# Kernel optimization log

Hardware: AMD Instinct MI355X
Metric: run time of the kernel (lower is better)

The kernel has to match this reference:

```python
import jax, jax.numpy as jnp
import numpy as np

N_NODES = 100000
N_EDGES = 1600000
IN_CH = 256
OUT_CH = 128
EPS = 1e-12


def setup_inputs() -> dict:
    key = jax.random.key(0)
    k1, k2, k3 = jax.random.split(key, 3)
    x = jax.random.normal(k1, (N_NODES, IN_CH), dtype=jnp.float32)
    edge_index = jax.random.randint(k2, (2, N_EDGES), 0, N_NODES, dtype=jnp.int64)
    W = jax.random.normal(k3, (IN_CH, OUT_CH), dtype=jnp.float32) / np.float32(np.sqrt(IN_CH))
    b = jnp.zeros((OUT_CH,), dtype=jnp.float32)
    return {"x": x, "edge_index": edge_index, "W": W, "b": b}


def reference(x, edge_index, W, b):
    n = x.shape[0]
    # GCNConv: linear transform first, then normalized aggregation with self-loops
    h = x @ W  # [N, out]
    loops = jnp.arange(n, dtype=edge_index.dtype)
    row = jnp.concatenate([edge_index[0], loops])  # source nodes
    col = jnp.concatenate([edge_index[1], loops])  # destination nodes
    deg = jax.ops.segment_sum(jnp.ones_like(col, dtype=h.dtype), col, num_segments=n)
    dinv = jnp.where(deg > 0, jax.lax.rsqrt(jnp.maximum(deg, 1.0)), 0.0)  # deg^-1/2, inf->0
    wgt = dinv[row] * dinv[col]  # symmetric normalization per edge
    agg = jax.ops.segment_sum(h[row] * wgt[:, None], col, num_segments=n) + b  # [N, out]
    # min-max scale per node (dim=1)
    zmin = agg.min(axis=1, keepdims=True)
    zmax = agg.max(axis=1, keepdims=True)
    z = (agg - zmin) / (zmax - zmin)
    # F.normalize: L2 along dim=1 with eps clamp
    nrm = jnp.maximum(jnp.linalg.norm(z, axis=1, keepdims=True), EPS)
    return z / nrm
```

## Files before the change

kernel.cpp:

```cpp
#include <hip/hip_runtime.h>
#include <hip/hip_bf16.h>

#define N_NODES 100000
#define N_EDGES 1600000
#define IN_CH 256
#define OUT_CH 128

#define BSZ 256
#define NBUCK 391
#define BCAP 4736
#define CSC 4096
#define SCB 391
#define PREPB 64

#define GEMM_ROWS 32
#define GEMB 3125

typedef __attribute__((ext_vector_type(8))) short short8;
typedef __attribute__((ext_vector_type(4))) float floatx4;
typedef __attribute__((ext_vector_type(2))) float float2v;

union bfu { __hip_bfloat16 b; unsigned short u; };

__device__ inline unsigned short f2bf(float v) {
    bfu cv; cv.b = __float2bfloat16(v); return cv.u;
}
__device__ inline float bf2f(unsigned short u) {
    bfu cv; cv.u = u; return __bfloat162float(cv.b);
}

__device__ inline void pkfma(float2v& acc, unsigned g, float2v dnp) {
    float2v v;
    v.x = __uint_as_float(g << 16);
    v.y = __uint_as_float(g & 0xffff0000u);
    asm("v_pk_fma_f32 %0, %1, %2, %3" : "=v"(acc) : "v"(v), "v"(dnp), "v"(acc));
}

__global__ __launch_bounds__(512) void k_init(const float* __restrict__ W,
                                              unsigned short* __restrict__ wb_hi,
                                              unsigned short* __restrict__ wb_lo,
                                              int* __restrict__ bcursor,
                                              unsigned* __restrict__ zrow) {
    int tid = threadIdx.x;
    if (blockIdx.x == 0 && tid < NBUCK) bcursor[tid] = 0;
    if (blockIdx.x == 1 && tid < 64) zrow[tid] = 0;

    int t = blockIdx.x * 512 + tid;
    int j = t & 7;
    int lane = (t >> 3) & 63;
    int s = (t >> 9) & 7;
    int nt = t >> 12;
    int k = s * 32 + (lane >> 4) * 8 + j;
    int n = nt * 16 + (lane & 15);
    float w = W[k * OUT_CH + n];
    unsigned short hi = f2bf(w);
    wb_hi[t] = hi;
    wb_lo[t] = f2bf(w - bf2f(hi));
}

__global__ __launch_bounds__(512) void k_main(const int* __restrict__ rows,
                                              const int* __restrict__ cols,
                                              int* __restrict__ bcursor,
                                              unsigned* __restrict__ ebuf,
                                              const float* __restrict__ x,
                                              const unsigned short* __restrict__ wb_hi,
                                              const unsigned short* __restrict__ wb_lo,
                                              unsigned short* __restrict__ hbs) {
    __shared__ int lcnt[NBUCK];
    __shared__ int lbase[NBUCK];
    __shared__ short8 xbh[2 * 8 * 68];
    __shared__ short8 xbl[2 * 8 * 68];

    int t = threadIdx.x;

    if (blockIdx.x < SCB) {
        if (t < NBUCK) lcnt[t] = 0;
        __syncthreads();

        int s0 = blockIdx.x * CSC;
        int e1 = min(N_EDGES, s0 + CSC);

        unsigned val[8];
        int bkr[8], rk[8];
#pragma unroll
        for (int u = 0; u < 8; ++u) {
            int i = s0 + t + u * 512;
            bool p = i < e1;
            int c = p ? cols[i] : 0;
            int r = p ? rows[i] : 0;
            int bk = c >> 8;
            bkr[u] = bk;
            val[u] = ((unsigned)(c & (BSZ - 1)) << 17) | (unsigned)r;
            rk[u] = p ? atomicAdd(&lcnt[bk], 1) : 0;
        }
        __syncthreads();
        if (t < NBUCK) {
            int c = lcnt[t];
            lbase[t] = c ? atomicAdd(&bcursor[t], c) : 0;
        }
        __syncthreads();
#pragma unroll
        for (int u = 0; u < 8; ++u) {
            int i = s0 + t + u * 512;
            if (i < e1) ebuf[bkr[u] * BCAP + lbase[bkr[u]] + rk[u]] = val[u];
        }
        return;
    }

    int wv = t >> 6;
    int lane = t & 63;
    int row0 = (blockIdx.x - SCB) * GEMM_ROWS;

    short8 Bh[8], Bl[8];
    const short8* bhp = (const short8*)wb_hi + (size_t)wv * 8 * 64 + lane;
    const short8* blp = (const short8*)wb_lo + (size_t)wv * 8 * 64 + lane;
#pragma unroll
    for (int s = 0; s < 8; ++s) {
        Bh[s] = bhp[s * 64];
        Bl[s] = blp[s * 64];
    }

#pragma unroll
    for (int q = 0; q < 2; ++q) {
        int c = q * 512 + t;
        int row = c >> 5;
        int cc  = c & 31;
        const float4* xp = (const float4*)(x + (size_t)(row0 + row) * IN_CH + cc * 8);
        float4 v0 = xp[0];
        float4 v1 = xp[1];
        float xv[8] = {v0.x, v0.y, v0.z, v0.w, v1.x, v1.y, v1.z, v1.w};
        short8 hh, ll;
#pragma unroll
        for (int j = 0; j < 8; ++j) {
            unsigned short hi = f2bf(xv[j]);
            hh[j] = (short)hi;
            ll[j] = (short)f2bf(xv[j] - bf2f(hi));
        }
        int ms = row >> 4, r15 = row & 15, s = cc >> 2, q2 = cc & 3;
        int idx = (ms * 8 + s) * 68 + q2 * 17 + r15;
        xbh[idx] = hh;
        xbl[idx] = ll;
    }
    __syncthreads();

    int r15 = lane & 15;
    int quad = lane >> 4;
    int lidx = quad * 17 + r15;

    floatx4 acc[2];
#pragma unroll
    for (int ms = 0; ms < 2; ++ms) {
        acc[ms] = (floatx4){0.f, 0.f, 0.f, 0.f};
#pragma unroll
        for (int s = 0; s < 8; ++s) {
            short8 ah = xbh[(ms * 8 + s) * 68 + lidx];
            short8 al = xbl[(ms * 8 + s) * 68 + lidx];
            acc[ms] = __builtin_amdgcn_mfma_f32_16x16x32_bf16(ah, Bh[s], acc[ms], 0, 0, 0);
            acc[ms] = __builtin_amdgcn_mfma_f32_16x16x32_bf16(ah, Bl[s], acc[ms], 0, 0, 0);
            acc[ms] = __builtin_amdgcn_mfma_f32_16x16x32_bf16(al, Bh[s], acc[ms], 0, 0, 0);
        }
    }

#pragma unroll
    for (int ms = 0; ms < 2; ++ms)
#pragma unroll
        for (int r = 0; r < 4; ++r) {
            int row = row0 + ms * 16 + quad * 4 + r;
            size_t idx = (size_t)row * OUT_CH + wv * 16 + r15;
            hbs[idx] = f2bf(acc[ms][r]);
        }
}

__global__ __launch_bounds__(512) void pb_build(const unsigned* __restrict__ ebuf,
                                                const int* __restrict__ bcursor,
                                                int* __restrict__ cnt,
                                                int* __restrict__ base,
                                                float* __restrict__ dinv,
                                                int* __restrict__ es) {
    __shared__ int nh[BSZ];
    __shared__ int sc[BSZ];
    int t = threadIdx.x;
    int bk = blockIdx.x;
    int bb = bk * BCAP;
    int bc = bcursor[bk];
    if (t < BSZ) nh[t] = 0;
    __syncthreads();

    unsigned val[10];
    int rk[10];
#pragma unroll
    for (int u = 0; u < 10; ++u) {
        int i = t + u * 512;
        bool p = i < bc;
        unsigned v = p ? ebuf[bb + i] : 0u;
        val[u] = v;
        rk[u] = p ? atomicAdd(&nh[v >> 17], 1) : 0;
    }
    __syncthreads();
    if (t < BSZ) sc[t] = nh[t];
    __syncthreads();
    for (int off = 1; off < BSZ; off <<= 1) {
        int v = (t < BSZ && t >= off) ? sc[t - off] : 0;
        __syncthreads();
        if (t < BSZ) sc[t] += v;
        __syncthreads();
    }
    if (t < BSZ) {
        int node = bk * BSZ + t;
        if (node < N_NODES) {
            int c = nh[t];
            cnt[node] = c;
            base[node] = bb + sc[t] - c;
            dinv[node] = rsqrtf((float)(c + 1));
        }
    }
#pragma unroll
    for (int u = 0; u < 10; ++u) {
        int i = t + u * 512;
        if (i < bc) {
            unsigned v = val[u];
            int dl = v >> 17;
            es[bb + sc[dl] - nh[dl] + rk[u]] = (int)(v & 0x1FFFFu) << 8;
        }
    }
}

__global__ __launch_bounds__(256) void k_agg_fin(const unsigned short* __restrict__ hbs,
                                                 const float* __restrict__ dinv,
                                                 const int* __restrict__ es,
                                                 const int* __restrict__ base,
                                                 const int* __restrict__ cnt,
                                                 const float* __restrict__ b,
                                                 float* __restrict__ out) {
    int t = threadIdx.x;
    int lane = t & 63;
    int ll = lane & 15;
    int node = blockIdx.x * 16 + (t >> 4);

    const char* hb = (const char*)hbs;
    const char* dvc = (const char*)dinv;
    int lane_byte = ll << 4;
    int bidx = (lane & 48) << 2;

    float dn = dinv[node];
    int d  = cnt[node];
    int st = base[node];

    float4 bv0 = ((const float4*)b)[ll * 2];
    float4 bv1 = ((const float4*)b)[ll * 2 + 1];

    uint4 gs = *(const uint4*)(hb + ((size_t)node << 8) + lane_byte);
    float2v dself; dself.x = dn; dself.y = dn;
    float2v acc[4];
#pragma unroll
    for (int c = 0; c < 4; ++c) { acc[c].x = 0.f; acc[c].y = 0.f; }
    pkfma(acc[0], gs.x, dself); pkfma(acc[1], gs.y, dself);
    pkfma(acc[2], gs.z, dself); pkfma(acc[3], gs.w, dself);

    int dm = d;
    dm = max(dm, __shfl_xor(dm, 16, 64));
    dm = max(dm, __shfl_xor(dm, 32, 64));
    int iters = __builtin_amdgcn_readfirstlane((dm + 15) >> 4);

    const int zoff = N_NODES << 8;

    int off = zoff; float dnv = 0.f;
    if (ll < d) {
        off = es[st + ll];
        dnv = *(const float*)(dvc + ((unsigned)off >> 6));
    }

    for (int it = 0; it < iters; ++it) {
        int offn = zoff; float dnn = 0.f;
        int jb2 = (it + 1) << 4;
        if (jb2 + ll < d) {
            offn = es[st + jb2 + ll];
            dnn = *(const float*)(dvc + ((unsigned)offn >> 6));
        }
        int dni = __float_as_int(dnv);

        uint4 ga[4], gb[4];
        float2v da[4], db[4];
#pragma unroll
        for (int k = 0; k < 4; ++k) {
            int ro = __builtin_amdgcn_ds_bpermute(bidx + (k << 2), off);
            float f = __int_as_float(__builtin_amdgcn_ds_bpermute(bidx + (k << 2), dni));
            da[k].x = f; da[k].y = f;
            ga[k] = *(const uint4*)(hb + (unsigned)(ro + lane_byte));
        }
#pragma unroll
        for (int k = 0; k < 4; ++k) {
            int ro = __builtin_amdgcn_ds_bpermute(bidx + ((4 + k) << 2), off);
            float f = __int_as_float(__builtin_amdgcn_ds_bpermute(bidx + ((4 + k) << 2), dni));
            db[k].x = f; db[k].y = f;
            gb[k] = *(const uint4*)(hb + (unsigned)(ro + lane_byte));
        }
#pragma unroll
        for (int k = 0; k < 4; ++k) {
            pkfma(acc[0], ga[k].x, da[k]); pkfma(acc[1], ga[k].y, da[k]);
            pkfma(acc[2], ga[k].z, da[k]); pkfma(acc[3], ga[k].w, da[k]);
        }
#pragma unroll
        for (int k = 0; k < 4; ++k) {
            int ro = __builtin_amdgcn_ds_bpermute(bidx + ((8 + k) << 2), off);
            float f = __int_as_float(__builtin_amdgcn_ds_bpermute(bidx + ((8 + k) << 2), dni));
            da[k].x = f; da[k].y = f;
            ga[k] = *(const uint4*)(hb + (unsigned)(ro + lane_byte));
        }
#pragma unroll
        for (int k = 0; k < 4; ++k) {
            pkfma(acc[0], gb[k].x, db[k]); pkfma(acc[1], gb[k].y, db[k]);
            pkfma(acc[2], gb[k].z, db[k]); pkfma(acc[3], gb[k].w, db[k]);
        }
#pragma unroll
        for (int k = 0; k < 4; ++k) {
            int ro = __builtin_amdgcn_ds_bpermute(bidx + ((12 + k) << 2), off);
            float f = __int_as_float(__builtin_amdgcn_ds_bpermute(bidx + ((12 + k) << 2), dni));
            db[k].x = f; db[k].y = f;
            gb[k] = *(const uint4*)(hb + (unsigned)(ro + lane_byte));
        }
#pragma unroll
        for (int k = 0; k < 4; ++k) {
            pkfma(acc[0], ga[k].x, da[k]); pkfma(acc[1], ga[k].y, da[k]);
            pkfma(acc[2], ga[k].z, da[k]); pkfma(acc[3], ga[k].w, da[k]);
        }
#pragma unroll
        for (int k = 0; k < 4; ++k) {
            pkfma(acc[0], gb[k].x, db[k]); pkfma(acc[1], gb[k].y, db[k]);
            pkfma(acc[2], gb[k].z, db[k]); pkfma(acc[3], gb[k].w, db[k]);
        }

        off = offn; dnv = dnn;
    }

    float v[8];
    v[0] = dn * acc[0].x + bv0.x;  v[1] = dn * acc[0].y + bv0.y;
    v[2] = dn * acc[1].x + bv0.z;  v[3] = dn * acc[1].y + bv0.w;
    v[4] = dn * acc[2].x + bv1.x;  v[5] = dn * acc[2].y + bv1.y;
    v[6] = dn * acc[3].x + bv1.z;  v[7] = dn * acc[3].y + bv1.w;

    float lmin = v[0], lmax = v[0];
#pragma unroll
    for (int i = 1; i < 8; ++i) { lmin = fminf(lmin, v[i]); lmax = fmaxf(lmax, v[i]); }
#pragma unroll
    for (int m = 8; m; m >>= 1) {
        lmin = fminf(lmin, __shfl_xor(lmin, m, 64));
        lmax = fmaxf(lmax, __shfl_xor(lmax, m, 64));
    }
    float scale = 1.0f / (lmax - lmin);
    float z[8];
    float ss = 0.f;
#pragma unroll
    for (int i = 0; i < 8; ++i) { z[i] = (v[i] - lmin) * scale; ss += z[i] * z[i]; }
#pragma unroll
    for (int m = 8; m; m >>= 1) ss += __shfl_xor(ss, m, 64);
    float inv = 1.0f / fmaxf(sqrtf(ss), 1e-12f);

    float4 o0 = {z[0] * inv, z[1] * inv, z[2] * inv, z[3] * inv};
    float4 o1 = {z[4] * inv, z[5] * inv, z[6] * inv, z[7] * inv};
    float4* op = (float4*)(out + (size_t)node * OUT_CH);
    op[ll * 2] = o0;
    op[ll * 2 + 1] = o1;
}

extern "C" void kernel_launch(void* const* d_in, const int* in_sizes, int n_in,
                              void* d_out, int out_size, void* d_ws, size_t ws_size,
                              hipStream_t stream) {
    const float* x = (const float*)d_in[0];
    const int* ei = (const int*)d_in[1];
    const float* W = (const float*)d_in[2];
    const float* b = (const float*)d_in[3];
    float* out = (float*)d_out;

    char* ws = (char*)d_ws;
    size_t o = 0;
    auto alloc = [&](size_t bytes) { void* p = ws + o; o = (o + bytes + 255) & ~(size_t)255; return p; };
    float* dinv    = (float*)alloc((size_t)N_NODES * 4);
    int*   cnt     = (int*)  alloc((size_t)N_NODES * 4);
    int*   base    = (int*)  alloc((size_t)N_NODES * 4);
    int*   bcursor = (int*)  alloc(NBUCK * 4);
    unsigned short* wb_hi = (unsigned short*)alloc((size_t)IN_CH * OUT_CH * 2);
    unsigned short* wb_lo = (unsigned short*)alloc((size_t)IN_CH * OUT_CH * 2);
    unsigned short* hbs = (unsigned short*)alloc((size_t)(N_NODES + 1) * OUT_CH * 2);
    unsigned* ebuf = (unsigned*)alloc((size_t)NBUCK * BCAP * 4);
    int*   es      = (int*)  alloc((size_t)NBUCK * BCAP * 4);

    const int* rows = ei;
    const int* cols = ei + N_EDGES;

    k_init<<<PREPB, 512, 0, stream>>>(W, wb_hi, wb_lo, bcursor,
                                      (unsigned*)(hbs + (size_t)N_NODES * OUT_CH));

    k_main<<<SCB + GEMB, 512, 0, stream>>>(rows, cols, bcursor, ebuf,
                                           x, wb_hi, wb_lo, hbs);

    pb_build<<<NBUCK, 512, 0, stream>>>(ebuf, bcursor, cnt, base, dinv, es);

    k_agg_fin<<<N_NODES / 16, 256, 0, stream>>>(hbs, dinv, es, base, cnt, b, out);
}
```

Baseline: 273.4 us.

## Fuse bucket sort into aggregation kernel with smaller buckets and global degree counts

```diff
diff --git a/kernel.cpp b/kernel.cpp
--- a/kernel.cpp
+++ b/kernel.cpp
@@ -6,9 +6,9 @@
 #define IN_CH 256
 #define OUT_CH 128
 
-#define BSZ 256
-#define NBUCK 391
-#define BCAP 4736
+#define BSZ 64
+#define NBUCK 1563
+#define BCAP 1408
 #define CSC 4096
 #define SCB 391
 #define PREPB 64
@@ -40,12 +40,16 @@
                                               unsigned short* __restrict__ wb_hi,
                                               unsigned short* __restrict__ wb_lo,
                                               int* __restrict__ bcursor,
+                                              int* __restrict__ cnt_g,
                                               unsigned* __restrict__ zrow) {
     int tid = threadIdx.x;
-    if (blockIdx.x == 0 && tid < NBUCK) bcursor[tid] = 0;
+    int g = blockIdx.x * 512 + tid;
+    if (blockIdx.x == 0)
+        for (int i = tid; i < NBUCK; i += 512) bcursor[i] = 0;
     if (blockIdx.x == 1 && tid < 64) zrow[tid] = 0;
-
-    int t = blockIdx.x * 512 + tid;
+    for (int i = g; i < N_NODES + 1; i += PREPB * 512) cnt_g[i] = 0;
+
+    int t = g;
     int j = t & 7;
     int lane = (t >> 3) & 63;
     int s = (t >> 9) & 7;
@@ -61,20 +65,19 @@
 __global__ __launch_bounds__(512) void k_main(const int* __restrict__ rows,
                                               const int* __restrict__ cols,
                                               int* __restrict__ bcursor,
+                                              int* __restrict__ cnt_g,
                                               unsigned* __restrict__ ebuf,
                                               const float* __restrict__ x,
                                               const unsigned short* __restrict__ wb_hi,
                                               const unsigned short* __restrict__ wb_lo,
                                               unsigned short* __restrict__ hbs) {
-    __shared__ int lcnt[NBUCK];
-    __shared__ int lbase[NBUCK];
-    __shared__ short8 xbh[2 * 8 * 68];
-    __shared__ short8 xbl[2 * 8 * 68];
-
+    __shared__ __align__(16) char smraw[34816];
     int t = threadIdx.x;
 
     if (blockIdx.x < SCB) {
-        if (t < NBUCK) lcnt[t] = 0;
+        int* lcnt  = (int*)smraw;
+        int* lbase = (int*)(smraw + 6272);
+        for (int i = t; i < NBUCK; i += 512) lcnt[i] = 0;
         __syncthreads();
 
         int s0 = blockIdx.x * CSC;
@@ -88,15 +91,16 @@
             bool p = i < e1;
             int c = p ? cols[i] : 0;
             int r = p ? rows[i] : 0;
-            int bk = c >> 8;
+            int bk = c >> 6;
             bkr[u] = bk;
             val[u] = ((unsigned)(c & (BSZ - 1)) << 17) | (unsigned)r;
             rk[u] = p ? atomicAdd(&lcnt[bk], 1) : 0;
+            if (p) atomicAdd(&cnt_g[c], 1);
         }
         __syncthreads();
-        if (t < NBUCK) {
-            int c = lcnt[t];
-            lbase[t] = c ? atomicAdd(&bcursor[t], c) : 0;
+        for (int i = t; i < NBUCK; i += 512) {
+            int c2 = lcnt[i];
+            lbase[i] = c2 ? atomicAdd(&bcursor[i], c2) : 0;
         }
         __syncthreads();
 #pragma unroll
@@ -107,6 +111,8 @@
         return;
     }
 
+    short8* xbh = (short8*)smraw;
+    short8* xbl = (short8*)(smraw + 17408);
     int wv = t >> 6;
     int lane = t & 63;
     int row0 = (blockIdx.x - SCB) * GEMM_ROWS;
@@ -171,25 +177,27 @@
         }
 }
 
-__global__ __launch_bounds__(512) void pb_build(const unsigned* __restrict__ ebuf,
-                                                const int* __restrict__ bcursor,
-                                                int* __restrict__ cnt,
-                                                int* __restrict__ base,
-                                                float* __restrict__ dinv,
-                                                int* __restrict__ es) {
+__global__ __launch_bounds__(512) void k_fin(const unsigned* __restrict__ ebuf,
+                                             const int* __restrict__ bcursor,
+                                             const int* __restrict__ cnt_g,
+                                             const unsigned short* __restrict__ hbs,
+                                             const float* __restrict__ b,
+                                             float* __restrict__ out) {
     __shared__ int nh[BSZ];
-    __shared__ int sc[BSZ];
+    __shared__ int sb[BSZ];
+    __shared__ int es_l[BCAP];
     int t = threadIdx.x;
     int bk = blockIdx.x;
     int bb = bk * BCAP;
     int bc = bcursor[bk];
+
     if (t < BSZ) nh[t] = 0;
     __syncthreads();
 
-    unsigned val[10];
-    int rk[10];
-#pragma unroll
-    for (int u = 0; u < 10; ++u) {
+    unsigned val[3];
+    int rk[3];
+#pragma unroll
+    for (int u = 0; u < 3; ++u) {
         int i = t + u * 512;
         bool p = i < bc;
         unsigned v = p ? ebuf[bb + i] : 0u;
@@ -197,170 +205,158 @@
         rk[u] = p ? atomicAdd(&nh[v >> 17], 1) : 0;
     }
     __syncthreads();
-    if (t < BSZ) sc[t] = nh[t];
-    __syncthreads();
-    for (int off = 1; off < BSZ; off <<= 1) {
-        int v = (t < BSZ && t >= off) ? sc[t - off] : 0;
-        __syncthreads();
-        if (t < BSZ) sc[t] += v;
-        __syncthreads();
-    }
-    if (t < BSZ) {
-        int node = bk * BSZ + t;
-        if (node < N_NODES) {
-            int c = nh[t];
-            cnt[node] = c;
-            base[node] = bb + sc[t] - c;
-            dinv[node] = rsqrtf((float)(c + 1));
-        }
-    }
-#pragma unroll
-    for (int u = 0; u < 10; ++u) {
+    if (t < 64) {
+        int s = nh[t];
+#pragma unroll
+        for (int d0 = 1; d0 < 64; d0 <<= 1) {
+            int u = __shfl_up(s, d0, 64);
+            if (t >= d0) s += u;
+        }
+        sb[t] = s - nh[t];
+    }
+    __syncthreads();
+#pragma unroll
+    for (int u = 0; u < 3; ++u) {
         int i = t + u * 512;
         if (i < bc) {
             unsigned v = val[u];
             int dl = v >> 17;
-            es[bb + sc[dl] - nh[dl] + rk[u]] = (int)(v & 0x1FFFFu) << 8;
-        }
-    }
-}
-
-__global__ __launch_bounds__(256) void k_agg_fin(const unsigned short* __restrict__ hbs,
-                                                 const float* __restrict__ dinv,
-                                                 const int* __restrict__ es,
-                                                 const int* __restrict__ base,
-                                                 const int* __restrict__ cnt,
-                                                 const float* __restrict__ b,
-                                                 float* __restrict__ out) {
-    int t = threadIdx.x;
+            es_l[sb[dl] + rk[u]] = (int)(v & 0x1FFFFu) << 8;
+        }
+    }
+    __syncthreads();
+
     int lane = t & 63;
     int ll = lane & 15;
-    int node = blockIdx.x * 16 + (t >> 4);
-
-    const char* hb = (const char*)hbs;
-    const char* dvc = (const char*)dinv;
     int lane_byte = ll << 4;
     int bidx = (lane & 48) << 2;
-
-    float dn = dinv[node];
-    int d  = cnt[node];
-    int st = base[node];
+    int grp = t >> 4;
+    const char* hb = (const char*)hbs;
+    const int zoff = N_NODES << 8;
 
     float4 bv0 = ((const float4*)b)[ll * 2];
     float4 bv1 = ((const float4*)b)[ll * 2 + 1];
 
-    uint4 gs = *(const uint4*)(hb + ((size_t)node << 8) + lane_byte);
-    float2v dself; dself.x = dn; dself.y = dn;
-    float2v acc[4];
-#pragma unroll
-    for (int c = 0; c < 4; ++c) { acc[c].x = 0.f; acc[c].y = 0.f; }
-    pkfma(acc[0], gs.x, dself); pkfma(acc[1], gs.y, dself);
-    pkfma(acc[2], gs.z, dself); pkfma(acc[3], gs.w, dself);
-
-    int dm = d;
-    dm = max(dm, __shfl_xor(dm, 16, 64));
-    dm = max(dm, __shfl_xor(dm, 32, 64));
-    int iters = __builtin_amdgcn_readfirstlane((dm + 15) >> 4);
-
-    const int zoff = N_NODES << 8;
-
-    int off = zoff; float dnv = 0.f;
-    if (ll < d) {
-        off = es[st + ll];
-        dnv = *(const float*)(dvc + ((unsigned)off >> 6));
-    }
-
-    for (int it = 0; it < iters; ++it) {
-        int offn = zoff; float dnn = 0.f;
-        int jb2 = (it + 1) << 4;
-        if (jb2 + ll < d) {
-            offn = es[st + jb2 + ll];
-            dnn = *(const float*)(dvc + ((unsigned)offn >> 6));
-        }
-        int dni = __float_as_int(dnv);
-
-        uint4 ga[4], gb[4];
-        float2v da[4], db[4];
-#pragma unroll
-        for (int k = 0; k < 4; ++k) {
-            int ro = __builtin_amdgcn_ds_bpermute(bidx + (k << 2), off);
-            float f = __int_as_float(__builtin_amdgcn_ds_bpermute(bidx + (k << 2), dni));
-            da[k].x = f; da[k].y = f;
-            ga[k] = *(const uint4*)(hb + (unsigned)(ro + lane_byte));
-        }
-#pragma unroll
-        for (int k = 0; k < 4; ++k) {
-            int ro = __builtin_amdgcn_ds_bpermute(bidx + ((4 + k) << 2), off);
-            float f = __int_as_float(__builtin_amdgcn_ds_bpermute(bidx + ((4 + k) << 2), dni));
-            db[k].x = f; db[k].y = f;
-            gb[k] = *(const uint4*)(hb + (unsigned)(ro + lane_byte));
-        }
-#pragma unroll
-        for (int k = 0; k < 4; ++k) {
-            pkfma(acc[0], ga[k].x, da[k]); pkfma(acc[1], ga[k].y, da[k]);
-            pkfma(acc[2], ga[k].z, da[k]); pkfma(acc[3], ga[k].w, da[k]);
-        }
-#pragma unroll
-        for (int k = 0; k < 4; ++k) {
-            int ro = __builtin_amdgcn_ds_bpermute(bidx + ((8 + k) << 2), off);
-            float f = __int_as_float(__builtin_amdgcn_ds_bpermute(bidx + ((8 + k) << 2), dni));
-            da[k].x = f; da[k].y = f;
-            ga[k] = *(const uint4*)(hb + (unsigned)(ro + lane_byte));
-        }
-#pragma unroll
-        for (int k = 0; k < 4; ++k) {
-            pkfma(acc[0], gb[k].x, db[k]); pkfma(acc[1], gb[k].y, db[k]);
-            pkfma(acc[2], gb[k].z, db[k]); pkfma(acc[3], gb[k].w, db[k]);
-        }
-#pragma unroll
-        for (int k = 0; k < 4; ++k) {
-            int ro = __builtin_amdgcn_ds_bpermute(bidx + ((12 + k) << 2), off);
-            float f = __int_as_float(__builtin_amdgcn_ds_bpermute(bidx + ((12 + k) << 2), dni));
-            db[k].x = f; db[k].y = f;
-            gb[k] = *(const uint4*)(hb + (unsigned)(ro + lane_byte));
-        }
-#pragma unroll
-        for (int k = 0; k < 4; ++k) {
-            pkfma(acc[0], ga[k].x, da[k]); pkfma(acc[1], ga[k].y, da[k]);
-            pkfma(acc[2], ga[k].z, da[k]); pkfma(acc[3], ga[k].w, da[k]);
-        }
-#pragma unroll
-        for (int k = 0; k < 4; ++k) {
-            pkfma(acc[0], gb[k].x, db[k]); pkfma(acc[1], gb[k].y, db[k]);
-            pkfma(acc[2], gb[k].z, db[k]); pkfma(acc[3], gb[k].w, db[k]);
-        }
-
-        off = offn; dnv = dnn;
-    }
-
-    float v[8];
-    v[0] = dn * acc[0].x + bv0.x;  v[1] = dn * acc[0].y + bv0.y;
-    v[2] = dn * acc[1].x + bv0.z;  v[3] = dn * acc[1].y + bv0.w;
-    v[4] = dn * acc[2].x + bv1.x;  v[5] = dn * acc[2].y + bv1.y;
-    v[6] = dn * acc[3].x + bv1.z;  v[7] = dn * acc[3].y + bv1.w;
-
-    float lmin = v[0], lmax = v[0];
-#pragma unroll
-    for (int i = 1; i < 8; ++i) { lmin = fminf(lmin, v[i]); lmax = fmaxf(lmax, v[i]); }
-#pragma unroll
-    for (int m = 8; m; m >>= 1) {
-        lmin = fminf(lmin, __shfl_xor(lmin, m, 64));
-        lmax = fmaxf(lmax, __shfl_xor(lmax, m, 64));
-    }
-    float scale = 1.0f / (lmax - lmin);
-    float z[8];
-    float ss = 0.f;
-#pragma unroll
-    for (int i = 0; i < 8; ++i) { z[i] = (v[i] - lmin) * scale; ss += z[i] * z[i]; }
-#pragma unroll
-    for (int m = 8; m; m >>= 1) ss += __shfl_xor(ss, m, 64);
-    float inv = 1.0f / fmaxf(sqrtf(ss), 1e-12f);
-
-    float4 o0 = {z[0] * inv, z[1] * inv, z[2] * inv, z[3] * inv};
-    float4 o1 = {z[4] * inv, z[5] * inv, z[6] * inv, z[7] * inv};
-    float4* op = (float4*)(out + (size_t)node * OUT_CH);
-    op[ll * 2] = o0;
-    op[ll * 2 + 1] = o1;
+    for (int r = 0; r < 2; ++r) {
+        int dl = r * 32 + grp;
+        int node = bk * BSZ + dl;
+        if (node >= N_NODES) break;
+
+        int d  = nh[dl];
+        int st0 = sb[dl];
+        float dn = rsqrtf((float)(d + 1));
+
+        uint4 gs = *(const uint4*)(hb + ((size_t)node << 8) + lane_byte);
+        float2v dself; dself.x = dn; dself.y = dn;
+        float2v acc[4];
+#pragma unroll
+        for (int c = 0; c < 4; ++c) { acc[c].x = 0.f; acc[c].y = 0.f; }
+        pkfma(acc[0], gs.x, dself); pkfma(acc[1], gs.y, dself);
+        pkfma(acc[2], gs.z, dself); pkfma(acc[3], gs.w, dself);
+
+        int dm = d;
+        dm = max(dm, __shfl_xor(dm, 16, 64));
+        dm = max(dm, __shfl_xor(dm, 32, 64));
+        int iters = __builtin_amdgcn_readfirstlane((dm + 15) >> 4);
+
+        int off = zoff; float dnv = 0.f;
+        if (ll < d) {
+            off = es_l[st0 + ll];
+            dnv = rsqrtf((float)(cnt_g[(unsigned)off >> 8] + 1));
+        }
+
+        for (int it = 0; it < iters; ++it) {
+            int offn = zoff; float dnn = 0.f;
+            int jb2 = (it + 1) << 4;
+            if (jb2 + ll < d) {
+                offn = es_l[st0 + jb2 + ll];
+                dnn = rsqrtf((float)(cnt_g[(unsigned)offn >> 8] + 1));
+            }
+            int dni = __float_as_int(dnv);
+
+            uint4 ga[4], gb[4];
+            float2v da[4], db[4];
+#pragma unroll
+            for (int k = 0; k < 4; ++k) {
+                int ro = __builtin_amdgcn_ds_bpermute(bidx + (k << 2), off);
+                float f = __int_as_float(__builtin_amdgcn_ds_bpermute(bidx + (k << 2), dni));
+                da[k].x = f; da[k].y = f;
+                ga[k] = *(const uint4*)(hb + (unsigned)(ro + lane_byte));
+            }
+#pragma unroll
+            for (int k = 0; k < 4; ++k) {
+                int ro = __builtin_amdgcn_ds_bpermute(bidx + ((4 + k) << 2), off);
+                float f = __int_as_float(__builtin_amdgcn_ds_bpermute(bidx + ((4 + k) << 2), dni));
+                db[k].x = f; db[k].y = f;
+                gb[k] = *(const uint4*)(hb + (unsigned)(ro + lane_byte));
+            }
+#pragma unroll
+            for (int k = 0; k < 4; ++k) {
+                pkfma(acc[0], ga[k].x, da[k]); pkfma(acc[1], ga[k].y, da[k]);
+                pkfma(acc[2], ga[k].z, da[k]); pkfma(acc[3], ga[k].w, da[k]);
+            }
+#pragma unroll
+            for (int k = 0; k < 4; ++k) {
+                int ro = __builtin_amdgcn_ds_bpermute(bidx + ((8 + k) << 2), off);
+                float f = __int_as_float(__builtin_amdgcn_ds_bpermute(bidx + ((8 + k) << 2), dni));
+                da[k].x = f; da[k].y = f;
+                ga[k] = *(const uint4*)(hb + (unsigned)(ro + lane_byte));
+            }
+#pragma unroll
+            for (int k = 0; k < 4; ++k) {
+                pkfma(acc[0], gb[k].x, db[k]); pkfma(acc[1], gb[k].y, db[k]);
+                pkfma(acc[2], gb[k].z, db[k]); pkfma(acc[3], gb[k].w, db[k]);
+            }
+#pragma unroll
+            for (int k = 0; k < 4; ++k) {
+                int ro = __builtin_amdgcn_ds_bpermute(bidx + ((12 + k) << 2), off);
+                float f = __int_as_float(__builtin_amdgcn_ds_bpermute(bidx + ((12 + k) << 2), dni));
+                db[k].x = f; db[k].y = f;
+                gb[k] = *(const uint4*)(hb + (unsigned)(ro + lane_byte));
+            }
+#pragma unroll
+            for (int k = 0; k < 4; ++k) {
+                pkfma(acc[0], ga[k].x, da[k]); pkfma(acc[1], ga[k].y, da[k]);
+                pkfma(acc[2], ga[k].z, da[k]); pkfma(acc[3], ga[k].w, da[k]);
+            }
+#pragma unroll
+            for (int k = 0; k < 4; ++k) {
+                pkfma(acc[0], gb[k].x, db[k]); pkfma(acc[1], gb[k].y, db[k]);
+                pkfma(acc[2], gb[k].z, db[k]); pkfma(acc[3], gb[k].w, db[k]);
+            }
+
+            off = offn; dnv = dnn;
+        }
+
+        float v[8];
+        v[0] = dn * acc[0].x + bv0.x;  v[1] = dn * acc[0].y + bv0.y;
+        v[2] = dn * acc[1].x + bv0.z;  v[3] = dn * acc[1].y + bv0.w;
+        v[4] = dn * acc[2].x + bv1.x;  v[5] = dn * acc[2].y + bv1.y;
+        v[6] = dn * acc[3].x + bv1.z;  v[7] = dn * acc[3].y + bv1.w;
+
+        float lmin = v[0], lmax = v[0];
+#pragma unroll
+        for (int i = 1; i < 8; ++i) { lmin = fminf(lmin, v[i]); lmax = fmaxf(lmax, v[i]); }
+#pragma unroll
+        for (int m = 8; m; m >>= 1) {
+            lmin = fminf(lmin, __shfl_xor(lmin, m, 64));
+            lmax = fmaxf(lmax, __shfl_xor(lmax, m, 64));
+        }
+        float scale = 1.0f / (lmax - lmin);
+        float z[8];
+        float ss = 0.f;
+#pragma unroll
+        for (int i = 0; i < 8; ++i) { z[i] = (v[i] - lmin) * scale; ss += z[i] * z[i]; }
+#pragma unroll
+        for (int m = 8; m; m >>= 1) ss += __shfl_xor(ss, m, 64);
+        float inv = 1.0f / fmaxf(sqrtf(ss), 1e-12f);
+
+        float4 o0 = {z[0] * inv, z[1] * inv, z[2] * inv, z[3] * inv};
+        float4 o1 = {z[4] * inv, z[5] * inv, z[6] * inv, z[7] * inv};
+        float4* op = (float4*)(out + (size_t)node * OUT_CH);
+        op[ll * 2] = o0;
+        op[ll * 2 + 1] = o1;
+    }
 }
 
 extern "C" void kernel_launch(void* const* d_in, const int* in_sizes, int n_in,
@@ -375,26 +371,21 @@
     char* ws = (char*)d_ws;
     size_t o = 0;
     auto alloc = [&](size_t bytes) { void* p = ws + o; o = (o + bytes + 255) & ~(size_t)255; return p; };
-    float* dinv    = (float*)alloc((size_t)N_NODES * 4);
-    int*   cnt     = (int*)  alloc((size_t)N_NODES * 4);
-    int*   base    = (int*)  alloc((size_t)N_NODES * 4);
-    int*   bcursor = (int*)  alloc(NBUCK * 4);
+    int*   bcursor = (int*)  alloc((size_t)NBUCK * 4);
+    int*   cnt_g   = (int*)  alloc((size_t)(N_NODES + 1) * 4);
     unsigned short* wb_hi = (unsigned short*)alloc((size_t)IN_CH * OUT_CH * 2);
     unsigned short* wb_lo = (unsigned short*)alloc((size_t)IN_CH * OUT_CH * 2);
     unsigned short* hbs = (unsigned short*)alloc((size_t)(N_NODES + 1) * OUT_CH * 2);
     unsigned* ebuf = (unsigned*)alloc((size_t)NBUCK * BCAP * 4);
-    int*   es      = (int*)  alloc((size_t)NBUCK * BCAP * 4);
 
     const int* rows = ei;
     const int* cols = ei + N_EDGES;
 
-    k_init<<<PREPB, 512, 0, stream>>>(W, wb_hi, wb_lo, bcursor,
+    k_init<<<PREPB, 512, 0, stream>>>(W, wb_hi, wb_lo, bcursor, cnt_g,
                                       (unsigned*)(hbs + (size_t)N_NODES * OUT_CH));
 
-    k_main<<<SCB + GEMB, 512, 0, stream>>>(rows, cols, bcursor, ebuf,
+    k_main<<<SCB + GEMB, 512, 0, stream>>>(rows, cols, bcursor, cnt_g, ebuf,
                                            x, wb_hi, wb_lo, hbs);
 
-    pb_build<<<NBUCK, 512, 0, stream>>>(ebuf, bcursor, cnt, base, dinv, es);
-
-    k_agg_fin<<<N_NODES / 16, 256, 0, stream>>>(hbs, dinv, es, base, cnt, b, out);
-}
+    k_fin<<<NBUCK, 512, 0, stream>>>(ebuf, bcursor, cnt_g, hbs, b, out);
+}
```

Measured after the change: 319.7 us. 16.9% more time.

## Split GEMM across scatter and bucket-build kernels to overlap phases

Applied to the files above, without the earlier changes.

```diff
diff --git a/kernel.cpp b/kernel.cpp
--- a/kernel.cpp
+++ b/kernel.cpp
@@ -14,7 +14,8 @@
 #define PREPB 64
 
 #define GEMM_ROWS 32
-#define GEMB 3125
+#define GEMMA 1024
+#define GEMMB 2101
 
 typedef __attribute__((ext_vector_type(8))) short short8;
 typedef __attribute__((ext_vector_type(4))) float floatx4;
@@ -34,6 +35,74 @@
     v.x = __uint_as_float(g << 16);
     v.y = __uint_as_float(g & 0xffff0000u);
     asm("v_pk_fma_f32 %0, %1, %2, %3" : "=v"(acc) : "v"(v), "v"(dnp), "v"(acc));
+}
+
+__device__ inline void gemm_body(const float* __restrict__ x,
+                                 const unsigned short* __restrict__ wb_hi,
+                                 const unsigned short* __restrict__ wb_lo,
+                                 unsigned short* __restrict__ hbs,
+                                 int row0, int t, short8* xbh, short8* xbl) {
+    int wv = t >> 6;
+    int lane = t & 63;
+
+    short8 Bh[8], Bl[8];
+    const short8* bhp = (const short8*)wb_hi + (size_t)wv * 8 * 64 + lane;
+    const short8* blp = (const short8*)wb_lo + (size_t)wv * 8 * 64 + lane;
+#pragma unroll
+    for (int s = 0; s < 8; ++s) {
+        Bh[s] = bhp[s * 64];
+        Bl[s] = blp[s * 64];
+    }
+
+#pragma unroll
+    for (int q = 0; q < 2; ++q) {
+        int c = q * 512 + t;
+        int row = c >> 5;
+        int cc  = c & 31;
+        const float4* xp = (const float4*)(x + (size_t)(row0 + row) * IN_CH + cc * 8);
+        float4 v0 = xp[0];
+        float4 v1 = xp[1];
+        float xv[8] = {v0.x, v0.y, v0.z, v0.w, v1.x, v1.y, v1.z, v1.w};
+        short8 hh, ll;
+#pragma unroll
+        for (int j = 0; j < 8; ++j) {
+            unsigned short hi = f2bf(xv[j]);
+            hh[j] = (short)hi;
+            ll[j] = (short)f2bf(xv[j] - bf2f(hi));
+        }
+        int ms = row >> 4, r15 = row & 15, s = cc >> 2, q2 = cc & 3;
+        int idx = (ms * 8 + s) * 68 + q2 * 17 + r15;
+        xbh[idx] = hh;
+        xbl[idx] = ll;
+    }
+    __syncthreads();
+
+    int r15 = lane & 15;
+    int quad = lane >> 4;
+    int lidx = quad * 17 + r15;
+
+    floatx4 acc[2];
+#pragma unroll
+    for (int ms = 0; ms < 2; ++ms) {
+        acc[ms] = (floatx4){0.f, 0.f, 0.f, 0.f};
+#pragma unroll
+        for (int s = 0; s < 8; ++s) {
+            short8 ah = xbh[(ms * 8 + s) * 68 + lidx];
+            short8 al = xbl[(ms * 8 + s) * 68 + lidx];
+            acc[ms] = __builtin_amdgcn_mfma_f32_16x16x32_bf16(ah, Bh[s], acc[ms], 0, 0, 0);
+            acc[ms] = __builtin_amdgcn_mfma_f32_16x16x32_bf16(ah, Bl[s], acc[ms], 0, 0, 0);
+            acc[ms] = __builtin_amdgcn_mfma_f32_16x16x32_bf16(al, Bh[s], acc[ms], 0, 0, 0);
+        }
+    }
+
+#pragma unroll
+    for (int ms = 0; ms < 2; ++ms)
+#pragma unroll
+        for (int r = 0; r < 4; ++r) {
+            int row = row0 + ms * 16 + quad * 4 + r;
+            size_t idx = (size_t)row * OUT_CH + wv * 16 + r15;
+            hbs[idx] = f2bf(acc[ms][r]);
+        }
 }
 
 __global__ __launch_bounds__(512) void k_init(const float* __restrict__ W,
@@ -58,19 +127,18 @@
     wb_lo[t] = f2bf(w - bf2f(hi));
 }
 
-__global__ __launch_bounds__(512) void k_main(const int* __restrict__ rows,
-                                              const int* __restrict__ cols,
-                                              int* __restrict__ bcursor,
-                                              unsigned* __restrict__ ebuf,
-                                              const float* __restrict__ x,
-                                              const unsigned short* __restrict__ wb_hi,
-                                              const unsigned short* __restrict__ wb_lo,
-                                              unsigned short* __restrict__ hbs) {
+__global__ __launch_bounds__(512) void k_mainA(const int* __restrict__ rows,
+                                               const int* __restrict__ cols,
+                                               int* __restrict__ bcursor,
+                                               unsigned* __restrict__ ebuf,
+                                               const float* __restrict__ x,
+                                               const unsigned short* __restrict__ wb_hi,
+                                               const unsigned short* __restrict__ wb_lo,
+                                               unsigned short* __restrict__ hbs) {
     __shared__ int lcnt[NBUCK];
     __shared__ int lbase[NBUCK];
     __shared__ short8 xbh[2 * 8 * 68];
     __shared__ short8 xbl[2 * 8 * 68];
-
     int t = threadIdx.x;
 
     if (blockIdx.x < SCB) {
@@ -95,8 +163,8 @@
         }
         __syncthreads();
         if (t < NBUCK) {
-            int c = lcnt[t];
-            lbase[t] = c ? atomicAdd(&bcursor[t], c) : 0;
+            int c2 = lcnt[t];
+            lbase[t] = c2 ? atomicAdd(&bcursor[t], c2) : 0;
         }
         __syncthreads();
 #pragma unroll
@@ -107,122 +175,74 @@
         return;
     }
 
-    int wv = t >> 6;
-    int lane = t & 63;
-    int row0 = (blockIdx.x - SCB) * GEMM_ROWS;
-
-    short8 Bh[8], Bl[8];
-    const short8* bhp = (const short8*)wb_hi + (size_t)wv * 8 * 64 + lane;
-    const short8* blp = (const short8*)wb_lo + (size_t)wv * 8 * 64 + lane;
-#pragma unroll
-    for (int s = 0; s < 8; ++s) {
-        Bh[s] = bhp[s * 64];
-        Bl[s] = blp[s * 64];
-    }
-
-#pragma unroll
-    for (int q = 0; q < 2; ++q) {
-        int c = q * 512 + t;
-        int row = c >> 5;
-        int cc  = c & 31;
-        const float4* xp = (const float4*)(x + (size_t)(row0 + row) * IN_CH + cc * 8);
-        float4 v0 = xp[0];
-        float4 v1 = xp[1];
-        float xv[8] = {v0.x, v0.y, v0.z, v0.w, v1.x, v1.y, v1.z, v1.w};
-        short8 hh, ll;
-#pragma unroll
-        for (int j = 0; j < 8; ++j) {
-            unsigned short hi = f2bf(xv[j]);
-            hh[j] = (short)hi;
-            ll[j] = (short)f2bf(xv[j] - bf2f(hi));
-        }
-        int ms = row >> 4, r15 = row & 15, s = cc >> 2, q2 = cc & 3;
-        int idx = (ms * 8 + s) * 68 + q2 * 17 + r15;
-        xbh[idx] = hh;
-        xbl[idx] = ll;
-    }
-    __syncthreads();
-
-    int r15 = lane & 15;
-    int quad = lane >> 4;
-    int lidx = quad * 17 + r15;
-
-    floatx4 acc[2];
-#pragma unroll
-    for (int ms = 0; ms < 2; ++ms) {
-        acc[ms] = (floatx4){0.f, 0.f, 0.f, 0.f};
-#pragma unroll
-        for (int s = 0; s < 8; ++s) {
-            short8 ah = xbh[(ms * 8 + s) * 68 + lidx];
-            short8 al = xbl[(ms * 8 + s) * 68 + lidx];
-            acc[ms] = __builtin_amdgcn_mfma_f32_16x16x32_bf16(ah, Bh[s], acc[ms], 0, 0, 0);
-            acc[ms] = __builtin_amdgcn_mfma_f32_16x16x32_bf16(ah, Bl[s], acc[ms], 0, 0, 0);
-            acc[ms] = __builtin_amdgcn_mfma_f32_16x16x32_bf16(al, Bh[s], acc[ms], 0, 0, 0);
-        }
-    }
-
-#pragma unroll
-    for (int ms = 0; ms < 2; ++ms)
-#pragma unroll
-        for (int r = 0; r < 4; ++r) {
-            int row = row0 + ms * 16 + quad * 4 + r;
-            size_t idx = (size_t)row * OUT_CH + wv * 16 + r15;
-            hbs[idx] = f2bf(acc[ms][r]);
-        }
-}
-
-__global__ __launch_bounds__(512) void pb_build(const unsigned* __restrict__ ebuf,
-                                                const int* __restrict__ bcursor,
-                                                int* __restrict__ cnt,
-                                                int* __restrict__ base,
-                                                float* __restrict__ dinv,
-                                                int* __restrict__ es) {
+    gemm_body(x, wb_hi, wb_lo, hbs, (int)(blockIdx.x - SCB) * GEMM_ROWS, t, xbh, xbl);
+}
+
+__global__ __launch_bounds__(512) void k_mainB(const unsigned* __restrict__ ebuf,
+                                               const int* __restrict__ bcursor,
+                                               int* __restrict__ cnt,
+                                               int* __restrict__ base,
+                                               float* __restrict__ dinv,
+                                               int* __restrict__ es,
+                                               const float* __restrict__ x,
+                                               const unsigned short* __restrict__ wb_hi,
+                                               const unsigned short* __restrict__ wb_lo,
+                                               unsigned short* __restrict__ hbs) {
     __shared__ int nh[BSZ];
     __shared__ int sc[BSZ];
+    __shared__ short8 xbh[2 * 8 * 68];
+    __shared__ short8 xbl[2 * 8 * 68];
     int t = threadIdx.x;
-    int bk = blockIdx.x;
-    int bb = bk * BCAP;
-    int bc = bcursor[bk];
-    if (t < BSZ) nh[t] = 0;
-    __syncthreads();
-
-    unsigned val[10];
-    int rk[10];
-#pragma unroll
-    for (int u = 0; u < 10; ++u) {
-        int i = t + u * 512;
-        bool p = i < bc;
-        unsigned v = p ? ebuf[bb + i] : 0u;
-        val[u] = v;
-        rk[u] = p ? atomicAdd(&nh[v >> 17], 1) : 0;
-    }
-    __syncthreads();
-    if (t < BSZ) sc[t] = nh[t];
-    __syncthreads();
-    for (int off = 1; off < BSZ; off <<= 1) {
-        int v = (t < BSZ && t >= off) ? sc[t - off] : 0;
-        __syncthreads();
-        if (t < BSZ) sc[t] += v;
-        __syncthreads();
-    }
-    if (t < BSZ) {
-        int node = bk * BSZ + t;
-        if (node < N_NODES) {
-            int c = nh[t];
-            cnt[node] = c;
-            base[node] = bb + sc[t] - c;
-            dinv[node] = rsqrtf((float)(c + 1));
-        }
-    }
-#pragma unroll
-    for (int u = 0; u < 10; ++u) {
-        int i = t + u * 512;
-        if (i < bc) {
-            unsigned v = val[u];
-            int dl = v >> 17;
-            es[bb + sc[dl] - nh[dl] + rk[u]] = (int)(v & 0x1FFFFu) << 8;
-        }
-    }
+
+    if (blockIdx.x < NBUCK) {
+        int bk = blockIdx.x;
+        int bb = bk * BCAP;
+        int bc = bcursor[bk];
+        if (t < BSZ) nh[t] = 0;
+        __syncthreads();
+
+        unsigned val[10];
+        int rk[10];
+#pragma unroll
+        for (int u = 0; u < 10; ++u) {
+            int i = t + u * 512;
+            bool p = i < bc;
+            unsigned v = p ? ebuf[bb + i] : 0u;
+            val[u] = v;
+            rk[u] = p ? atomicAdd(&nh[v >> 17], 1) : 0;
+        }
+        __syncthreads();
+        if (t < BSZ) sc[t] = nh[t];
+        __syncthreads();
+        for (int off = 1; off < BSZ; off <<= 1) {
+            int v = (t < BSZ && t >= off) ? sc[t - off] : 0;
+            __syncthreads();
+            if (t < BSZ) sc[t] += v;
+            __syncthreads();
+        }
+        if (t < BSZ) {
+            int node = bk * BSZ + t;
+            if (node < N_NODES) {
+                int c = nh[t];
+                cnt[node] = c;
+                base[node] = bb + sc[t] - c;
+                dinv[node] = rsqrtf((float)(c + 1));
+            }
+        }
+#pragma unroll
+        for (int u = 0; u < 10; ++u) {
+            int i = t + u * 512;
+            if (i < bc) {
+                unsigned v = val[u];
+                int dl = v >> 17;
+                es[bb + sc[dl] - nh[dl] + rk[u]] = (int)(v & 0x1FFFFu) << 8;
+            }
+        }
+        return;
+    }
+
+    gemm_body(x, wb_hi, wb_lo, hbs,
+              32768 + (int)(blockIdx.x - NBUCK) * GEMM_ROWS, t, xbh, xbl);
 }
 
 __global__ __launch_bounds__(256) void k_agg_fin(const unsigned short* __restrict__ hbs,
@@ -378,7 +398,7 @@
     float* dinv    = (float*)alloc((size_t)N_NODES * 4);
     int*   cnt     = (int*)  alloc((size_t)N_NODES * 4);
     int*   base    = (int*)  alloc((size_t)N_NODES * 4);
-    int*   bcursor = (int*)  alloc(NBUCK * 4);
+    int*   bcursor = (int*)  alloc((size_t)NBUCK * 4);
     unsigned short* wb_hi = (unsigned short*)alloc((size_t)IN_CH * OUT_CH * 2);
     unsigned short* wb_lo = (unsigned short*)alloc((size_t)IN_CH * OUT_CH * 2);
     unsigned short* hbs = (unsigned short*)alloc((size_t)(N_NODES + 1) * OUT_CH * 2);
@@ -391,10 +411,11 @@
     k_init<<<PREPB, 512, 0, stream>>>(W, wb_hi, wb_lo, bcursor,
                                       (unsigned*)(hbs + (size_t)N_NODES * OUT_CH));
 
-    k_main<<<SCB + GEMB, 512, 0, stream>>>(rows, cols, bcursor, ebuf,
-                                           x, wb_hi, wb_lo, hbs);
-
-    pb_build<<<NBUCK, 512, 0, stream>>>(ebuf, bcursor, cnt, base, dinv, es);
+    k_mainA<<<SCB + GEMMA, 512, 0, stream>>>(rows, cols, bcursor, ebuf,
+                                             x, wb_hi, wb_lo, hbs);
+
+    k_mainB<<<NBUCK + GEMMB, 512, 0, stream>>>(ebuf, bcursor, cnt, base, dinv, es,
+                                               x, wb_hi, wb_lo, hbs);
 
     k_agg_fin<<<N_NODES / 16, 256, 0, stream>>>(hbs, dinv, es, base, cnt, b, out);
 }
```

Measured after the change: 270.4 us. No clear change (-1.1%).
